# Kernel tuning notes

Measured on AMD Instinct MI355X. Metric: run time of the kernel, lower is better.

Reference implementation:

```python
import jax, jax.numpy as jnp
import numpy as np

IMG = 224          # image_size
FMAP = (56, 56)    # feature_map_dims (AdaptiveAvgPool2d((56,56)))
K_REWEIGHT = 3     # self.n_reweight
BLUR_RADIUS = 4    # KNNGaussianBlur(4): kernel 9, sigma 4


def _cdist(a, b):
    # Euclidean pairwise distance, [Na, D] x [Nb, D] -> [Na, Nb]
    a2 = jnp.sum(a * a, axis=1, keepdims=True)            # [Na,1]
    b2 = jnp.sum(b * b, axis=1, keepdims=True).T          # [1,Nb]
    d2 = a2 + b2 - 2.0 * (a @ b.T)
    return jnp.sqrt(jnp.maximum(d2, 0.0))


def _gaussian_blur(x):
    # x: [1,1,H,W]; torchvision GaussianBlur(kernel=9, sigma=4), reflect pad
    r, sigma = BLUR_RADIUS, float(BLUR_RADIUS)
    t = jnp.arange(2 * r + 1, dtype=x.dtype) - r
    g = jnp.exp(-(t * t) / (2.0 * sigma * sigma))
    g = g / jnp.sum(g)
    k2d = jnp.outer(g, g)[None, None]                     # [1,1,9,9]
    xp = jnp.pad(x, ((0, 0), (0, 0), (r, r), (r, r)), mode='reflect')
    return jax.lax.conv_general_dilated(
        xp, k2d, window_strides=(1, 1), padding='VALID',
        dimension_numbers=('NCHW', 'OIHW', 'NCHW'))


def setup_inputs() -> dict:
    key = jax.random.key(0)
    k1, k2 = jax.random.split(key)
    patch = jax.random.normal(k1, (FMAP[0] * FMAP[1], 768), dtype=jnp.float32)
    patch_lib = jax.random.normal(k2, (16384, 768), dtype=jnp.float32)
    mean = jnp.zeros((), dtype=jnp.float32)
    std = jnp.ones((), dtype=jnp.float32)
    return {"patch": patch, "patch_lib": patch_lib, "mean": mean, "std": std}


def reference(patch, patch_lib, mean, std):
    # normalization (method_name != 'Point_MAE' branch)
    p = (patch - mean) / std                               # [N, D]

    dist = _cdist(p, patch_lib)                            # [N, Nlib]
    min_val = jnp.min(dist, axis=1)                        # [N]
    min_idx = jnp.argmin(dist, axis=1)                     # [N]
    s_idx = jnp.argmax(min_val)
    s_star = jnp.max(min_val)

    m_test = p[s_idx]                                      # [D]
    m_star = patch_lib[min_idx[s_idx]]                     # [D]

    # distances of m_star to whole bank, k smallest
    w_dist = jnp.sqrt(jnp.maximum(
        jnp.sum((patch_lib - m_star) ** 2, axis=1), 0.0))  # [Nlib]
    _, nn_idx = jax.lax.top_k(-w_dist, K_REWEIGHT)         # smallest k
    m_star_knn = jnp.linalg.norm(
        m_test[None, :] - patch_lib[nn_idx[1:]], axis=1)   # [k-1]

    D_sqrt = jnp.sqrt(jnp.asarray(patch.shape[1], dtype=p.dtype))
    w = 1.0 - jnp.exp(s_star / D_sqrt) / jnp.sum(jnp.exp(m_star_knn / D_sqrt))
    s = w * s_star

    s_map = min_val.reshape(1, 1, *FMAP)
    s_map = jax.image.resize(s_map, (1, 1, IMG, IMG), method='bilinear')
    s_map = _gaussian_blur(s_map)
    return s, s_map
```

## Files before the change

### kernel.cpp

```cpp
#include <hip/hip_runtime.h>
#include <hip/hip_bf16.h>
#include <stdint.h>

#define N_PATCH 3136
#define N_PATCH_PAD 3200
#define N_LIB   16384
#define DIM     768
#define IMGSZ   224
#define FM      56

#define BK 32
#define KT 24
#define MT 25
#define NTILES 128

typedef __bf16 bf16_t;
typedef __bf16 bf16x8 __attribute__((ext_vector_type(8)));
typedef __bf16 bf16x4_v __attribute__((ext_vector_type(4)));
typedef float  f32x4  __attribute__((ext_vector_type(4)));

#define FLT_MAX_ 3.402823466e+38f

struct Scal {
  unsigned long long approx_max_pack;
  unsigned long long cand_pack[64];
  int cand[64];
  int cand_count;
  int done1;
};

__device__ __forceinline__ float wave_reduce_sum(float v) {
#pragma unroll
  for (int s = 32; s > 0; s >>= 1) v += __shfl_xor(v, s, 64);
  return v;
}

__device__ __forceinline__ unsigned long long shfl_xor_u64(unsigned long long v, int mask) {
  unsigned lo = (unsigned)v, hi = (unsigned)(v >> 32);
  lo = __shfl_xor(lo, mask, 64);
  hi = __shfl_xor(hi, mask, 64);
  return ((unsigned long long)hi << 32) | lo;
}

__device__ __forceinline__ void async16(const bf16_t* g, bf16_t* l) {
  __builtin_amdgcn_global_load_lds(
      (const __attribute__((address_space(1))) unsigned int*)g,
      (__attribute__((address_space(3))) unsigned int*)l, 16, 0, 0);
}

__global__ void prep_kernel(const float* __restrict__ patch, const float* __restrict__ lib,
                            const float* __restrict__ meanp, const float* __restrict__ stdp,
                            bf16_t* __restrict__ pb, bf16_t* __restrict__ lb,
                            float* __restrict__ a2, float* __restrict__ b2, Scal* sc) {
  int t = threadIdx.x;
  int lane = t & 63;
  if (blockIdx.x == 0) {
    if (t < 64) sc->cand_pack[t] = ~0ULL;
    if (t == 64) { sc->approx_max_pack = 0ULL; sc->cand_count = 0; sc->done1 = 0; }
  }
  if (blockIdx.x < N_PATCH / 4) {
    int row = blockIdx.x * 4 + (t >> 6);
    float mu = meanp[0], sd = stdp[0];
    float acc = 0.f;
#pragma unroll
    for (int k = 0; k < 3; k++) {
      float4 v = ((const float4*)(patch + (size_t)row * DIM))[lane + 64 * k];
      v.x = (v.x - mu) / sd; v.y = (v.y - mu) / sd;
      v.z = (v.z - mu) / sd; v.w = (v.w - mu) / sd;
      bf16x4_v o = {(__bf16)v.x, (__bf16)v.y, (__bf16)v.z, (__bf16)v.w};
      *(bf16x4_v*)(pb + (size_t)row * DIM + (lane + 64 * k) * 4) = o;
      acc += v.x*v.x + v.y*v.y + v.z*v.z + v.w*v.w;
    }
    acc = wave_reduce_sum(acc);
    if (lane == 0) a2[row] = acc;
  } else {
    int row = (blockIdx.x - N_PATCH / 4) * 4 + (t >> 6);
    float acc = 0.f;
#pragma unroll
    for (int k = 0; k < 3; k++) {
      float4 v = ((const float4*)(lib + (size_t)row * DIM))[lane + 64 * k];
      bf16x4_v o = {(__bf16)v.x, (__bf16)v.y, (__bf16)v.z, (__bf16)v.w};
      *(bf16x4_v*)(lb + (size_t)row * DIM + (lane + 64 * k) * 4) = o;
      acc += v.x*v.x + v.y*v.y + v.z*v.z + v.w*v.w;
    }
    acc = wave_reduce_sum(acc);
    if (lane == 0) b2[row] = acc;
  }
}

__global__ __launch_bounds__(256, 3)
void gemm_min_kernel(const bf16_t* __restrict__ pb, const bf16_t* __restrict__ lb,
                     const float* __restrict__ a2, const float* __restrict__ b2,
                     float* __restrict__ part) {
  __shared__ __align__(16) bf16_t As[2][128 * BK];
  __shared__ __align__(16) bf16_t Bs[2][128 * BK];
  __shared__ unsigned smin[128];

  const int t = threadIdx.x;
  const int wave = t >> 6;
  const int lane = t & 63;
  const int l15 = lane & 15;
  const int quad = lane >> 4;
  const int wm = (wave >> 1) * 64;
  const int wn = (wave & 1) * 64;

  const int lid = blockIdx.x;
  const int xcd = lid & 7;
  const int slot = lid >> 3;
  const int ntile = xcd + 8 * (slot / MT);
  const int mtile = slot % MT;
  const int m0 = mtile * 128;
  const int n0 = ntile * 128;

  int ra0 = m0 + (t >> 2);       if (ra0 > N_PATCH - 1) ra0 = N_PATCH - 1;
  int ra1 = m0 + 64 + (t >> 2);  if (ra1 > N_PATCH - 1) ra1 = N_PATCH - 1;
  const bf16_t* gA0 = pb + (size_t)ra0 * DIM + (t & 3) * 8;
  const bf16_t* gA1 = pb + (size_t)ra1 * DIM + (t & 3) * 8;
  const bf16_t* gB0 = lb + (size_t)(n0 + (t >> 2)) * DIM + (t & 3) * 8;
  const bf16_t* gB1 = gB0 + (size_t)64 * DIM;

  if (t < 128) smin[t] = 0xffffffffu;

  {
    bf16_t* la = &As[0][0];
    bf16_t* lb_ = &Bs[0][0];
    async16(gA0, la + t * 8);
    async16(gA1, la + 2048 + t * 8);
    async16(gB0, lb_ + t * 8);
    async16(gB1, lb_ + 2048 + t * 8);
  }
  __syncthreads();

  f32x4 acc[4][4];
#pragma unroll
  for (int mi = 0; mi < 4; mi++)
#pragma unroll
    for (int ni = 0; ni < 4; ni++) { f32x4 z = {0.f,0.f,0.f,0.f}; acc[mi][ni] = z; }

  for (int k = 0; k < KT; ++k) {
    const int cur = k & 1;
    if (k + 1 < KT) {
      const int nxt = cur ^ 1;
      const size_t ko = (size_t)(k + 1) * BK;
      bf16_t* la = &As[nxt][0];
      bf16_t* lb_ = &Bs[nxt][0];
      async16(gA0 + ko, la + t * 8);
      async16(gA1 + ko, la + 2048 + t * 8);
      async16(gB0 + ko, lb_ + t * 8);
      async16(gB1 + ko, lb_ + 2048 + t * 8);
    }

    bf16x8 afr[4], bfr[4];
#pragma unroll
    for (int mi = 0; mi < 4; mi++)
      afr[mi] = *(const bf16x8*)(&As[cur][(wm + mi * 16 + l15) * BK + quad * 8]);
#pragma unroll
    for (int ni = 0; ni < 4; ni++)
      bfr[ni] = *(const bf16x8*)(&Bs[cur][(wn + ni * 16 + l15) * BK + quad * 8]);
#pragma unroll
    for (int mi = 0; mi < 4; mi++)
#pragma unroll
      for (int ni = 0; ni < 4; ni++)
        acc[mi][ni] = __builtin_amdgcn_mfma_f32_16x16x32_bf16(afr[mi], bfr[ni],
                                                              acc[mi][ni], 0, 0, 0);
    __syncthreads();
  }

  float b2n[4];
#pragma unroll
  for (int ni = 0; ni < 4; ni++) b2n[ni] = b2[n0 + wn + ni * 16 + l15];

#pragma unroll
  for (int mi = 0; mi < 4; mi++) {
#pragma unroll
    for (int r = 0; r < 4; r++) {
      int rloc = wm + mi * 16 + quad * 4 + r;
      int mrow = m0 + rloc;
      float a2v = a2[mrow < N_PATCH ? mrow : (N_PATCH - 1)];
      float best = a2v + b2n[0] - 2.0f * acc[mi][0][r];
#pragma unroll
      for (int ni = 1; ni < 4; ni++)
        best = fminf(best, a2v + b2n[ni] - 2.0f * acc[mi][ni][r]);
      best = fmaxf(best, 0.0f);
#pragma unroll
      for (int s = 1; s < 16; s <<= 1)
        best = fminf(best, __shfl_xor(best, s, 64));
      if (l15 == 0) atomicMin(&smin[rloc], __float_as_uint(best));
    }
  }
  __syncthreads();
  if (t < 128) part[(size_t)ntile * N_PATCH_PAD + m0 + t] = __uint_as_float(smin[t]);
}

__global__ void finalize_collect_kernel(const float* __restrict__ part,
                                        float* __restrict__ min_val, Scal* sc) {
  __shared__ bool last;
  int t = threadIdx.x;
  int row = blockIdx.x * 128 + t;
  float m = FLT_MAX_;
#pragma unroll 8
  for (int nt = 0; nt < NTILES; nt++)
    m = fminf(m, part[(size_t)nt * N_PATCH_PAD + row]);
  if (row < N_PATCH) {
    float v = sqrtf(m);
    min_val[row] = v;
    unsigned long long mp = (((unsigned long long)__float_as_uint(v)) << 32) |
                            (unsigned)(0xffffffffu - (unsigned)row);
    atomicMax(&sc->approx_max_pack, mp);
  }
  __threadfence();
  __syncthreads();
  if (t == 0) last = (atomicAdd(&sc->done1, 1) == MT - 1);
  __syncthreads();
  if (!last) return;
  __threadfence();
  float amax = __uint_as_float((unsigned)(atomicMax(&sc->approx_max_pack, 0ULL) >> 32));
  for (int i = t; i < N_PATCH; i += 128) {
    if (min_val[i] >= amax - 0.02f) {
      int p = atomicAdd(&sc->cand_count, 1);
      if (p < 64) sc->cand[p] = i;
    }
  }
}

__global__ void refine_kernel(const float* __restrict__ patch, const float* __restrict__ lib,
                              const float* __restrict__ meanp, const float* __restrict__ stdp,
                              Scal* sc) {
  int c = blockIdx.x;
  int cnt = sc->cand_count; if (cnt > 64) cnt = 64;
  if (c >= cnt) return;
  int row = sc->cand[c];
  int wave = threadIdx.x >> 6, lane = threadIdx.x & 63;
  float mu = meanp[0], sd = stdp[0];
  float4 pv[3];
#pragma unroll
  for (int k = 0; k < 3; k++) {
    float4 v = ((const float4*)(patch + (size_t)row * DIM))[lane + 64 * k];
    v.x = (v.x - mu) / sd; v.y = (v.y - mu) / sd;
    v.z = (v.z - mu) / sd; v.w = (v.w - mu) / sd;
    pv[k] = v;
  }
  unsigned long long best = ~0ULL;
  int jbase = blockIdx.y * 128 + wave * 32;
  for (int rr = 0; rr < 32; rr++) {
    int j = jbase + rr;
    const float4* pl = (const float4*)(lib + (size_t)j * DIM);
    float acc = 0.f;
#pragma unroll
    for (int k = 0; k < 3; k++) {
      float4 l = pl[lane + 64 * k];
      float dx = pv[k].x - l.x, dy = pv[k].y - l.y;
      float dz = pv[k].z - l.z, dw = pv[k].w - l.w;
      acc += dx*dx + dy*dy + dz*dz + dw*dw;
    }
    acc = wave_reduce_sum(acc);
    unsigned long long pk = (((unsigned long long)__float_as_uint(acc)) << 32) | (unsigned)j;
    if (pk < best) best = pk;
  }
  if (lane == 0) atomicMin(&sc->cand_pack[c], best);
}

__device__ __forceinline__ void wave_pick(const Scal* sc, int lane,
                                          int* srow, float* sstar, int* ms) {
  int cnt = sc->cand_count; if (cnt > 64) cnt = 64;
  unsigned long long pk = 0ULL;
  int rowv = 0, msv = 0;
  if (lane < cnt) {
    unsigned long long cp = sc->cand_pack[lane];
    rowv = sc->cand[lane];
    msv = (int)(cp & 0xffffffffu);
    pk = (cp & 0xffffffff00000000ULL) | (unsigned)(0xffffffffu - (unsigned)rowv);
  }
  unsigned long long m = pk;
#pragma unroll
  for (int s = 1; s < 64; s <<= 1) {
    unsigned long long o = shfl_xor_u64(m, s);
    if (o > m) m = o;
  }
  unsigned long long mask = __ballot(pk == m && lane < cnt);
  int wl = (int)(__ffsll((long long)mask) - 1);
  *srow = __shfl(rowv, wl, 64);
  *ms   = __shfl(msv, wl, 64);
  *sstar = sqrtf(__uint_as_float((unsigned)(m >> 32)));
}

__global__ void wdist_kernel(const float* __restrict__ lib, const Scal* __restrict__ sc,
                             float* __restrict__ wdist2) {
  int wave = threadIdx.x >> 6, lane = threadIdx.x & 63;
  int srow_, ms; float ss_;
  wave_pick(sc, lane, &srow_, &ss_, &ms);
  float4 pm[3];
#pragma unroll
  for (int k = 0; k < 3; k++)
    pm[k] = ((const float4*)(lib + (size_t)ms * DIM))[lane + 64 * k];
  int jbase = blockIdx.x * 64 + wave * 16;
  for (int rr = 0; rr < 16; rr++) {
    int j = jbase + rr;
    const float4* pj = (const float4*)(lib + (size_t)j * DIM);
    float acc = 0.f;
#pragma unroll
    for (int k = 0; k < 3; k++) {
      float4 a = pj[lane + 64 * k];
      float dx = a.x - pm[k].x, dy = a.y - pm[k].y;
      float dz = a.z - pm[k].z, dw = a.w - pm[k].w;
      acc += dx*dx + dy*dy + dz*dz + dw*dw;
    }
    acc = wave_reduce_sum(acc);
    if (lane == 0) wdist2[j] = acc;
  }
}

__global__ void top3_kernel(const float* __restrict__ wdist2,
                            const float* __restrict__ patch, const float* __restrict__ lib,
                            const float* __restrict__ meanp, const float* __restrict__ stdp,
                            const Scal* __restrict__ sc, float* __restrict__ out) {
  __shared__ unsigned long long sl[768];
  int t = threadIdx.x;

  unsigned long long b0 = ~0ULL, b1 = ~0ULL, b2 = ~0ULL;
  for (int j = t; j < N_LIB; j += 256) {
    unsigned long long pk = (((unsigned long long)__float_as_uint(wdist2[j])) << 32) | (unsigned)j;
    if (pk < b0)      { b2 = b1; b1 = b0; b0 = pk; }
    else if (pk < b1) { b2 = b1; b1 = pk; }
    else if (pk < b2) { b2 = pk; }
  }
  sl[t * 3 + 0] = b0; sl[t * 3 + 1] = b1; sl[t * 3 + 2] = b2;
  __syncthreads();
  if (t >= 64) return;

  unsigned long long c0 = ~0ULL, c1 = ~0ULL, c2 = ~0ULL;
#pragma unroll
  for (int e = 0; e < 12; e++) {
    unsigned long long pk = sl[t * 12 + e];
    if (pk < c0)      { c2 = c1; c1 = c0; c0 = pk; }
    else if (pk < c1) { c2 = c1; c1 = pk; }
    else if (pk < c2) { c2 = pk; }
  }
  unsigned long long res1 = 0, res2 = 0;
#pragma unroll
  for (int r = 0; r < 3; r++) {
    unsigned long long m = c0;
#pragma unroll
    for (int s = 1; s < 64; s <<= 1) {
      unsigned long long o = shfl_xor_u64(m, s);
      if (o < m) m = o;
    }
    if (r == 1) res1 = m;
    if (r == 2) res2 = m;
    if (c0 == m) { c0 = c1; c1 = c2; c2 = ~0ULL; }
  }
  int nA = (int)(res1 & 0xffffffffu);
  int nB = (int)(res2 & 0xffffffffu);

  int srow, ms2; float sstar;
  wave_pick(sc, t, &srow, &sstar, &ms2);

  float mu = meanp[0], sd = stdp[0];
  float accA = 0.f, accB = 0.f;
#pragma unroll
  for (int k = 0; k < 3; k++) {
    float4 p4 = ((const float4*)(patch + (size_t)srow * DIM))[t + 64 * k];
    float4 a4 = ((const float4*)(lib + (size_t)nA * DIM))[t + 64 * k];
    float4 b4 = ((const float4*)(lib + (size_t)nB * DIM))[t + 64 * k];
    float px = (p4.x - mu) / sd, py = (p4.y - mu) / sd;
    float pz = (p4.z - mu) / sd, pw = (p4.w - mu) / sd;
    float dax = px - a4.x, day = py - a4.y, daz = pz - a4.z, daw = pw - a4.w;
    float dbx = px - b4.x, dby = py - b4.y, dbz = pz - b4.z, dbw = pw - b4.w;
    accA += dax*dax + day*day + daz*daz + daw*daw;
    accB += dbx*dbx + dby*dby + dbz*dbz + dbw*dbw;
  }
  accA = wave_reduce_sum(accA);
  accB = wave_reduce_sum(accB);
  if (t == 0) {
    float dsq = sqrtf((float)DIM);
    float d1 = sqrtf(accA), d2v = sqrtf(accB);
    float w = 1.0f - expf(sstar / dsq) / (expf(d1 / dsq) + expf(d2v / dsq));
    out[0] = w * sstar;
  }
}

__global__ void resize_blur_kernel(const float* __restrict__ mv, float* __restrict__ out) {
  __shared__ float rs[40 * 40];
  int bx = blockIdx.x % 7, by = blockIdx.x / 7;
  int ox0 = bx * 32, oy0 = by * 32;
  int t = threadIdx.x;

  for (int i = t; i < 1600; i += 256) {
    int ly = i / 40, lx = i % 40;
    int gy = oy0 - 4 + ly; gy = gy < 0 ? 0 : (gy > 223 ? 223 : gy);
    int gx = ox0 - 4 + lx; gx = gx < 0 ? 0 : (gx > 223 ? 223 : gx);
    float sy = fminf(fmaxf(0.25f * gy - 0.375f, 0.0f), 55.0f);
    float sx = fminf(fmaxf(0.25f * gx - 0.375f, 0.0f), 55.0f);
    int y0 = (int)sy; if (y0 > 54) y0 = 54;
    int x0 = (int)sx; if (x0 > 54) x0 = 54;
    float fy = sy - y0, fx = sx - x0;
    float v00 = mv[y0*FM + x0],     v01 = mv[y0*FM + x0 + 1];
    float v10 = mv[(y0+1)*FM + x0], v11 = mv[(y0+1)*FM + x0 + 1];
    float a = v00 + fx * (v01 - v00);
    float b = v10 + fx * (v11 - v10);
    rs[i] = a + fy * (b - a);
  }
  __syncthreads();

  float g[9]; float gs = 0.f;
#pragma unroll
  for (int i = 0; i < 9; i++) { float tt = (float)(i - 4); g[i] = expf(-(tt*tt)/32.0f); gs += g[i]; }
#pragma unroll
  for (int i = 0; i < 9; i++) g[i] /= gs;

  for (int p = t; p < 1024; p += 256) {
    int y = oy0 + p / 32, x = ox0 + (p & 31);
    float acc = 0.f;
#pragma unroll
    for (int dy = 0; dy < 9; dy++) {
      int yy = y + dy - 4;
      yy = yy < 0 ? -yy : (yy > IMGSZ - 1 ? 2*(IMGSZ-1) - yy : yy);
      int lyy = yy - (oy0 - 4);
      float ra = 0.f;
#pragma unroll
      for (int dx = 0; dx < 9; dx++) {
        int xx = x + dx - 4;
        xx = xx < 0 ? -xx : (xx > IMGSZ - 1 ? 2*(IMGSZ-1) - xx : xx);
        ra += g[dx] * rs[lyy * 40 + (xx - (ox0 - 4))];
      }
      acc += g[dy] * ra;
    }
    out[y * IMGSZ + x] = acc;
  }
}

extern "C" void kernel_launch(void* const* d_in, const int* in_sizes, int n_in,
                              void* d_out, int out_size, void* d_ws, size_t ws_size,
                              hipStream_t stream) {
  const float* patch = (const float*)d_in[0];
  const float* lib   = (const float*)d_in[1];
  const float* meanp = (const float*)d_in[2];
  const float* stdp  = (const float*)d_in[3];
  float* out = (float*)d_out;

  char* ws = (char*)d_ws;
  size_t off = 0;
  auto alloc = [&](size_t bytes) -> void* {
    void* p = ws + off;
    off = (off + bytes + 255) & ~(size_t)255;
    return p;
  };
  bf16_t* pb      = (bf16_t*)alloc((size_t)N_PATCH * DIM * sizeof(bf16_t));
  bf16_t* lb      = (bf16_t*)alloc((size_t)N_LIB * DIM * sizeof(bf16_t));
  float* a2       = (float*)alloc(N_PATCH * sizeof(float));
  float* b2       = (float*)alloc(N_LIB * sizeof(float));
  float* part     = (float*)alloc((size_t)N_PATCH_PAD * NTILES * sizeof(float));
  float* min_val  = (float*)alloc(N_PATCH * sizeof(float));
  float* wdist2   = (float*)alloc(N_LIB * sizeof(float));
  Scal*  sc       = (Scal*)alloc(sizeof(Scal));

  prep_kernel<<<N_PATCH / 4 + N_LIB / 4, 256, 0, stream>>>(patch, lib, meanp, stdp,
                                                           pb, lb, a2, b2, sc);
  gemm_min_kernel<<<MT * NTILES, 256, 0, stream>>>(pb, lb, a2, b2, part);
  finalize_collect_kernel<<<MT, 128, 0, stream>>>(part, min_val, sc);
  refine_kernel<<<dim3(64, 128), 256, 0, stream>>>(patch, lib, meanp, stdp, sc);
  wdist_kernel<<<256, 256, 0, stream>>>(lib, sc, wdist2);
  top3_kernel<<<1, 256, 0, stream>>>(wdist2, patch, lib, meanp, stdp, sc, out);
  resize_blur_kernel<<<49, 256, 0, stream>>>(min_val, out + 1);
}
```

Baseline: 367.5 us.

## Fuse post-GEMM tail kernels into one persistent kernel with grid barriers

Replaces five separate tail launches (finalize/collect, refine, wdist, top3, resize+blur) with a single 64-block kernel. The stages are separated by atomic-counter grid barriers kept in the Scal struct, whose counters prep_kernel resets. This targets the per-launch and inter-kernel gap overhead of the small tail stages. In exchange, the refine and wdist scans run on only 64 blocks instead of thousands or 256, which lowers memory-level parallelism for the library sweeps. Correctness relies on all 64 blocks being co-resident.

```diff
diff --git a/kernel.cpp b/kernel.cpp
--- a/kernel.cpp
+++ b/kernel.cpp
@@ -14,6 +14,8 @@
 #define MT 25
 #define NTILES 128
 
+#define TAILB 64
+
 typedef __bf16 bf16_t;
 typedef __bf16 bf16x8 __attribute__((ext_vector_type(8)));
 typedef __bf16 bf16x4_v __attribute__((ext_vector_type(4)));
@@ -26,7 +28,7 @@
   unsigned long long cand_pack[64];
   int cand[64];
   int cand_count;
-  int done1;
+  int bar[4];
 };
 
 __device__ __forceinline__ float wave_reduce_sum(float v) {
@@ -46,6 +48,17 @@
   __builtin_amdgcn_global_load_lds(
       (const __attribute__((address_space(1))) unsigned int*)g,
       (__attribute__((address_space(3))) unsigned int*)l, 16, 0, 0);
+}
+
+__device__ __forceinline__ void grid_bar(int* ctr, int nb) {
+  __syncthreads();
+  if (threadIdx.x == 0) {
+    __threadfence();
+    atomicAdd(ctr, 1);
+    while (atomicAdd(ctr, 0) < nb) __builtin_amdgcn_s_sleep(8);
+    __threadfence();
+  }
+  __syncthreads();
 }
 
 __global__ void prep_kernel(const float* __restrict__ patch, const float* __restrict__ lib,
@@ -56,7 +69,8 @@
   int lane = t & 63;
   if (blockIdx.x == 0) {
     if (t < 64) sc->cand_pack[t] = ~0ULL;
-    if (t == 64) { sc->approx_max_pack = 0ULL; sc->cand_count = 0; sc->done1 = 0; }
+    if (t == 64) { sc->approx_max_pack = 0ULL; sc->cand_count = 0; }
+    if (t >= 65 && t < 69) sc->bar[t - 65] = 0;
   }
   if (blockIdx.x < N_PATCH / 4) {
     int row = blockIdx.x * 4 + (t >> 6);
@@ -192,77 +206,8 @@
   if (t < 128) part[(size_t)ntile * N_PATCH_PAD + m0 + t] = __uint_as_float(smin[t]);
 }
 
-__global__ void finalize_collect_kernel(const float* __restrict__ part,
-                                        float* __restrict__ min_val, Scal* sc) {
-  __shared__ bool last;
-  int t = threadIdx.x;
-  int row = blockIdx.x * 128 + t;
-  float m = FLT_MAX_;
-#pragma unroll 8
-  for (int nt = 0; nt < NTILES; nt++)
-    m = fminf(m, part[(size_t)nt * N_PATCH_PAD + row]);
-  if (row < N_PATCH) {
-    float v = sqrtf(m);
-    min_val[row] = v;
-    unsigned long long mp = (((unsigned long long)__float_as_uint(v)) << 32) |
-                            (unsigned)(0xffffffffu - (unsigned)row);
-    atomicMax(&sc->approx_max_pack, mp);
-  }
-  __threadfence();
-  __syncthreads();
-  if (t == 0) last = (atomicAdd(&sc->done1, 1) == MT - 1);
-  __syncthreads();
-  if (!last) return;
-  __threadfence();
-  float amax = __uint_as_float((unsigned)(atomicMax(&sc->approx_max_pack, 0ULL) >> 32));
-  for (int i = t; i < N_PATCH; i += 128) {
-    if (min_val[i] >= amax - 0.02f) {
-      int p = atomicAdd(&sc->cand_count, 1);
-      if (p < 64) sc->cand[p] = i;
-    }
-  }
-}
-
-__global__ void refine_kernel(const float* __restrict__ patch, const float* __restrict__ lib,
-                              const float* __restrict__ meanp, const float* __restrict__ stdp,
-                              Scal* sc) {
-  int c = blockIdx.x;
-  int cnt = sc->cand_count; if (cnt > 64) cnt = 64;
-  if (c >= cnt) return;
-  int row = sc->cand[c];
-  int wave = threadIdx.x >> 6, lane = threadIdx.x & 63;
-  float mu = meanp[0], sd = stdp[0];
-  float4 pv[3];
-#pragma unroll
-  for (int k = 0; k < 3; k++) {
-    float4 v = ((const float4*)(patch + (size_t)row * DIM))[lane + 64 * k];
-    v.x = (v.x - mu) / sd; v.y = (v.y - mu) / sd;
-    v.z = (v.z - mu) / sd; v.w = (v.w - mu) / sd;
-    pv[k] = v;
-  }
-  unsigned long long best = ~0ULL;
-  int jbase = blockIdx.y * 128 + wave * 32;
-  for (int rr = 0; rr < 32; rr++) {
-    int j = jbase + rr;
-    const float4* pl = (const float4*)(lib + (size_t)j * DIM);
-    float acc = 0.f;
-#pragma unroll
-    for (int k = 0; k < 3; k++) {
-      float4 l = pl[lane + 64 * k];
-      float dx = pv[k].x - l.x, dy = pv[k].y - l.y;
-      float dz = pv[k].z - l.z, dw = pv[k].w - l.w;
-      acc += dx*dx + dy*dy + dz*dz + dw*dw;
-    }
-    acc = wave_reduce_sum(acc);
-    unsigned long long pk = (((unsigned long long)__float_as_uint(acc)) << 32) | (unsigned)j;
-    if (pk < best) best = pk;
-  }
-  if (lane == 0) atomicMin(&sc->cand_pack[c], best);
-}
-
-__device__ __forceinline__ void wave_pick(const Scal* sc, int lane,
+__device__ __forceinline__ void wave_pick(const Scal* sc, int cnt, int lane,
                                           int* srow, float* sstar, int* ms) {
-  int cnt = sc->cand_count; if (cnt > 64) cnt = 64;
   unsigned long long pk = 0ULL;
   int rowv = 0, msv = 0;
   if (lane < cnt) {
@@ -284,148 +229,224 @@
   *sstar = sqrtf(__uint_as_float((unsigned)(m >> 32)));
 }
 
-__global__ void wdist_kernel(const float* __restrict__ lib, const Scal* __restrict__ sc,
-                             float* __restrict__ wdist2) {
-  int wave = threadIdx.x >> 6, lane = threadIdx.x & 63;
-  int srow_, ms; float ss_;
-  wave_pick(sc, lane, &srow_, &ss_, &ms);
-  float4 pm[3];
-#pragma unroll
-  for (int k = 0; k < 3; k++)
-    pm[k] = ((const float4*)(lib + (size_t)ms * DIM))[lane + 64 * k];
-  int jbase = blockIdx.x * 64 + wave * 16;
-  for (int rr = 0; rr < 16; rr++) {
-    int j = jbase + rr;
-    const float4* pj = (const float4*)(lib + (size_t)j * DIM);
-    float acc = 0.f;
+__global__ __launch_bounds__(256, 2)
+void tail_kernel(const float* __restrict__ part, float* __restrict__ min_val,
+                 const float* __restrict__ patch, const float* __restrict__ lib,
+                 const float* __restrict__ meanp, const float* __restrict__ stdp,
+                 Scal* __restrict__ sc, float* __restrict__ wdist2,
+                 float* __restrict__ out0, float* __restrict__ outmap) {
+  __shared__ union {
+    unsigned long long sl[768];
+    float rs[40 * 40];
+  } sm;
+  __shared__ int s_cnt;
+
+  const int t = threadIdx.x;
+  const int b = blockIdx.x;
+  const int wave = t >> 6, lane = t & 63;
+
+  {
+    int row = b * 256 + t;
+    if (row < N_PATCH) {
+      float m = FLT_MAX_;
+#pragma unroll 8
+      for (int nt = 0; nt < NTILES; nt++)
+        m = fminf(m, part[(size_t)nt * N_PATCH_PAD + row]);
+      float v = sqrtf(m);
+      min_val[row] = v;
+      unsigned long long mp = (((unsigned long long)__float_as_uint(v)) << 32) |
+                              (unsigned)(0xffffffffu - (unsigned)row);
+      atomicMax(&sc->approx_max_pack, mp);
+    }
+  }
+  grid_bar(&sc->bar[0], TAILB);
+
+  if (b == 0) {
+    float amax = __uint_as_float((unsigned)(atomicMax(&sc->approx_max_pack, 0ULL) >> 32));
+    for (int i = t; i < N_PATCH; i += 256) {
+      if (min_val[i] >= amax - 0.02f) {
+        int p = atomicAdd(&sc->cand_count, 1);
+        if (p < 64) sc->cand[p] = i;
+      }
+    }
+  }
+  grid_bar(&sc->bar[1], TAILB);
+
+  if (t == 0) s_cnt = atomicAdd(&sc->cand_count, 0);
+  __syncthreads();
+  int cnt = s_cnt; if (cnt > 64) cnt = 64;
+
+  {
+    float mu = meanp[0], sd = stdp[0];
+    for (int c = 0; c < cnt; c++) {
+      int row = sc->cand[c];
+      float4 pv[3];
+#pragma unroll
+      for (int k = 0; k < 3; k++) {
+        float4 v = ((const float4*)(patch + (size_t)row * DIM))[lane + 64 * k];
+        v.x = (v.x - mu) / sd; v.y = (v.y - mu) / sd;
+        v.z = (v.z - mu) / sd; v.w = (v.w - mu) / sd;
+        pv[k] = v;
+      }
+      unsigned long long best = ~0ULL;
+      int jbase = b * 256 + wave * 64;
+      for (int rr = 0; rr < 64; rr++) {
+        int j = jbase + rr;
+        const float4* pl = (const float4*)(lib + (size_t)j * DIM);
+        float acc = 0.f;
+#pragma unroll
+        for (int k = 0; k < 3; k++) {
+          float4 l = pl[lane + 64 * k];
+          float dx = pv[k].x - l.x, dy = pv[k].y - l.y;
+          float dz = pv[k].z - l.z, dw = pv[k].w - l.w;
+          acc += dx*dx + dy*dy + dz*dz + dw*dw;
+        }
+        acc = wave_reduce_sum(acc);
+        unsigned long long pk = (((unsigned long long)__float_as_uint(acc)) << 32) | (unsigned)j;
+        if (pk < best) best = pk;
+      }
+      if (lane == 0) atomicMin(&sc->cand_pack[c], best);
+    }
+  }
+  grid_bar(&sc->bar[2], TAILB);
+
+  {
+    int srow_, ms; float ss_;
+    wave_pick(sc, cnt, lane, &srow_, &ss_, &ms);
+    float4 pm[3];
+#pragma unroll
+    for (int k = 0; k < 3; k++)
+      pm[k] = ((const float4*)(lib + (size_t)ms * DIM))[lane + 64 * k];
+    int jbase = b * 256 + wave * 64;
+    for (int rr = 0; rr < 64; rr++) {
+      int j = jbase + rr;
+      const float4* pj = (const float4*)(lib + (size_t)j * DIM);
+      float acc = 0.f;
+#pragma unroll
+      for (int k = 0; k < 3; k++) {
+        float4 a = pj[lane + 64 * k];
+        float dx = a.x - pm[k].x, dy = a.y - pm[k].y;
+        float dz = a.z - pm[k].z, dw = a.w - pm[k].w;
+        acc += dx*dx + dy*dy + dz*dz + dw*dw;
+      }
+      acc = wave_reduce_sum(acc);
+      if (lane == 0) wdist2[j] = acc;
+    }
+  }
+  grid_bar(&sc->bar[3], TAILB);
+
+  if (b == 0) {
+    unsigned long long b0 = ~0ULL, b1 = ~0ULL, b2 = ~0ULL;
+    for (int j = t; j < N_LIB; j += 256) {
+      unsigned long long pk = (((unsigned long long)__float_as_uint(wdist2[j])) << 32) | (unsigned)j;
+      if (pk < b0)      { b2 = b1; b1 = b0; b0 = pk; }
+      else if (pk < b1) { b2 = b1; b1 = pk; }
+      else if (pk < b2) { b2 = pk; }
+    }
+    sm.sl[t * 3 + 0] = b0; sm.sl[t * 3 + 1] = b1; sm.sl[t * 3 + 2] = b2;
+    __syncthreads();
+    if (t >= 64) return;
+
+    unsigned long long c0 = ~0ULL, c1 = ~0ULL, c2 = ~0ULL;
+#pragma unroll
+    for (int e = 0; e < 12; e++) {
+      unsigned long long pk = sm.sl[t * 12 + e];
+      if (pk < c0)      { c2 = c1; c1 = c0; c0 = pk; }
+      else if (pk < c1) { c2 = c1; c1 = pk; }
+      else if (pk < c2) { c2 = pk; }
+    }
+    unsigned long long res1 = 0, res2 = 0;
+#pragma unroll
+    for (int r = 0; r < 3; r++) {
+      unsigned long long m = c0;
+#pragma unroll
+      for (int s = 1; s < 64; s <<= 1) {
+        unsigned long long o = shfl_xor_u64(m, s);
+        if (o < m) m = o;
+      }
+      if (r == 1) res1 = m;
+      if (r == 2) res2 = m;
+      if (c0 == m) { c0 = c1; c1 = c2; c2 = ~0ULL; }
+    }
+    int nA = (int)(res1 & 0xffffffffu);
+    int nB = (int)(res2 & 0xffffffffu);
+
+    int srow, ms2; float sstar;
+    wave_pick(sc, cnt, t, &srow, &sstar, &ms2);
+
+    float mu = meanp[0], sd = stdp[0];
+    float accA = 0.f, accB = 0.f;
 #pragma unroll
     for (int k = 0; k < 3; k++) {
-      float4 a = pj[lane + 64 * k];
-      float dx = a.x - pm[k].x, dy = a.y - pm[k].y;
-      float dz = a.z - pm[k].z, dw = a.w - pm[k].w;
-      acc += dx*dx + dy*dy + dz*dz + dw*dw;
-    }
-    acc = wave_reduce_sum(acc);
-    if (lane == 0) wdist2[j] = acc;
-  }
-}
-
-__global__ void top3_kernel(const float* __restrict__ wdist2,
-                            const float* __restrict__ patch, const float* __restrict__ lib,
-                            const float* __restrict__ meanp, const float* __restrict__ stdp,
-                            const Scal* __restrict__ sc, float* __restrict__ out) {
-  __shared__ unsigned long long sl[768];
-  int t = threadIdx.x;
-
-  unsigned long long b0 = ~0ULL, b1 = ~0ULL, b2 = ~0ULL;
-  for (int j = t; j < N_LIB; j += 256) {
-    unsigned long long pk = (((unsigned long long)__float_as_uint(wdist2[j])) << 32) | (unsigned)j;
-    if (pk < b0)      { b2 = b1; b1 = b0; b0 = pk; }
-    else if (pk < b1) { b2 = b1; b1 = pk; }
-    else if (pk < b2) { b2 = pk; }
-  }
-  sl[t * 3 + 0] = b0; sl[t * 3 + 1] = b1; sl[t * 3 + 2] = b2;
-  __syncthreads();
-  if (t >= 64) return;
-
-  unsigned long long c0 = ~0ULL, c1 = ~0ULL, c2 = ~0ULL;
-#pragma unroll
-  for (int e = 0; e < 12; e++) {
-    unsigned long long pk = sl[t * 12 + e];
-    if (pk < c0)      { c2 = c1; c1 = c0; c0 = pk; }
-    else if (pk < c1) { c2 = c1; c1 = pk; }
-    else if (pk < c2) { c2 = pk; }
-  }
-  unsigned long long res1 = 0, res2 = 0;
-#pragma unroll
-  for (int r = 0; r < 3; r++) {
-    unsigned long long m = c0;
-#pragma unroll
-    for (int s = 1; s < 64; s <<= 1) {
-      unsigned long long o = shfl_xor_u64(m, s);
-      if (o < m) m = o;
-    }
-    if (r == 1) res1 = m;
-    if (r == 2) res2 = m;
-    if (c0 == m) { c0 = c1; c1 = c2; c2 = ~0ULL; }
-  }
-  int nA = (int)(res1 & 0xffffffffu);
-  int nB = (int)(res2 & 0xffffffffu);
-
-  int srow, ms2; float sstar;
-  wave_pick(sc, t, &srow, &sstar, &ms2);
-
-  float mu = meanp[0], sd = stdp[0];
-  float accA = 0.f, accB = 0.f;
-#pragma unroll
-  for (int k = 0; k < 3; k++) {
-    float4 p4 = ((const float4*)(patch + (size_t)srow * DIM))[t + 64 * k];
-    float4 a4 = ((const float4*)(lib + (size_t)nA * DIM))[t + 64 * k];
-    float4 b4 = ((const float4*)(lib + (size_t)nB * DIM))[t + 64 * k];
-    float px = (p4.x - mu) / sd, py = (p4.y - mu) / sd;
-    float pz = (p4.z - mu) / sd, pw = (p4.w - mu) / sd;
-    float dax = px - a4.x, day = py - a4.y, daz = pz - a4.z, daw = pw - a4.w;
-    float dbx = px - b4.x, dby = py - b4.y, dbz = pz - b4.z, dbw = pw - b4.w;
-    accA += dax*dax + day*day + daz*daz + daw*daw;
-    accB += dbx*dbx + dby*dby + dbz*dbz + dbw*dbw;
-  }
-  accA = wave_reduce_sum(accA);
-  accB = wave_reduce_sum(accB);
-  if (t == 0) {
-    float dsq = sqrtf((float)DIM);
-    float d1 = sqrtf(accA), d2v = sqrtf(accB);
-    float w = 1.0f - expf(sstar / dsq) / (expf(d1 / dsq) + expf(d2v / dsq));
-    out[0] = w * sstar;
-  }
-}
-
-__global__ void resize_blur_kernel(const float* __restrict__ mv, float* __restrict__ out) {
-  __shared__ float rs[40 * 40];
-  int bx = blockIdx.x % 7, by = blockIdx.x / 7;
-  int ox0 = bx * 32, oy0 = by * 32;
-  int t = threadIdx.x;
-
-  for (int i = t; i < 1600; i += 256) {
-    int ly = i / 40, lx = i % 40;
-    int gy = oy0 - 4 + ly; gy = gy < 0 ? 0 : (gy > 223 ? 223 : gy);
-    int gx = ox0 - 4 + lx; gx = gx < 0 ? 0 : (gx > 223 ? 223 : gx);
-    float sy = fminf(fmaxf(0.25f * gy - 0.375f, 0.0f), 55.0f);
-    float sx = fminf(fmaxf(0.25f * gx - 0.375f, 0.0f), 55.0f);
-    int y0 = (int)sy; if (y0 > 54) y0 = 54;
-    int x0 = (int)sx; if (x0 > 54) x0 = 54;
-    float fy = sy - y0, fx = sx - x0;
-    float v00 = mv[y0*FM + x0],     v01 = mv[y0*FM + x0 + 1];
-    float v10 = mv[(y0+1)*FM + x0], v11 = mv[(y0+1)*FM + x0 + 1];
-    float a = v00 + fx * (v01 - v00);
-    float b = v10 + fx * (v11 - v10);
-    rs[i] = a + fy * (b - a);
-  }
-  __syncthreads();
-
-  float g[9]; float gs = 0.f;
-#pragma unroll
-  for (int i = 0; i < 9; i++) { float tt = (float)(i - 4); g[i] = expf(-(tt*tt)/32.0f); gs += g[i]; }
-#pragma unroll
-  for (int i = 0; i < 9; i++) g[i] /= gs;
-
-  for (int p = t; p < 1024; p += 256) {
-    int y = oy0 + p / 32, x = ox0 + (p & 31);
-    float acc = 0.f;
-#pragma unroll
-    for (int dy = 0; dy < 9; dy++) {
-      int yy = y + dy - 4;
-      yy = yy < 0 ? -yy : (yy > IMGSZ - 1 ? 2*(IMGSZ-1) - yy : yy);
-      int lyy = yy - (oy0 - 4);
-      float ra = 0.f;
-#pragma unroll
-      for (int dx = 0; dx < 9; dx++) {
-        int xx = x + dx - 4;
-        xx = xx < 0 ? -xx : (xx > IMGSZ - 1 ? 2*(IMGSZ-1) - xx : xx);
-        ra += g[dx] * rs[lyy * 40 + (xx - (ox0 - 4))];
-      }
-      acc += g[dy] * ra;
-    }
-    out[y * IMGSZ + x] = acc;
+      float4 p4 = ((const float4*)(patch + (size_t)srow * DIM))[t + 64 * k];
+      float4 a4 = ((const float4*)(lib + (size_t)nA * DIM))[t + 64 * k];
+      float4 b4 = ((const float4*)(lib + (size_t)nB * DIM))[t + 64 * k];
+      float px = (p4.x - mu) / sd, py = (p4.y - mu) / sd;
+      float pz = (p4.z - mu) / sd, pw = (p4.w - mu) / sd;
+      float dax = px - a4.x, day = py - a4.y, daz = pz - a4.z, daw = pw - a4.w;
+      float dbx = px - b4.x, dby = py - b4.y, dbz = pz - b4.z, dbw = pw - b4.w;
+      accA += dax*dax + day*day + daz*daz + daw*daw;
+      accB += dbx*dbx + dby*dby + dbz*dbz + dbw*dbw;
+    }
+    accA = wave_reduce_sum(accA);
+    accB = wave_reduce_sum(accB);
+    if (t == 0) {
+      float dsq = sqrtf((float)DIM);
+      float d1 = sqrtf(accA), d2v = sqrtf(accB);
+      float w = 1.0f - expf(sstar / dsq) / (expf(d1 / dsq) + expf(d2v / dsq));
+      out0[0] = w * sstar;
+    }
+    return;
+  }
+
+  if (b > 49) return;
+  {
+    int tile = b - 1;
+    int bx = tile % 7, by = tile / 7;
+    int ox0 = bx * 32, oy0 = by * 32;
+
+    for (int i = t; i < 1600; i += 256) {
+      int ly = i / 40, lx = i % 40;
+      int gy = oy0 - 4 + ly; gy = gy < 0 ? 0 : (gy > 223 ? 223 : gy);
+      int gx = ox0 - 4 + lx; gx = gx < 0 ? 0 : (gx > 223 ? 223 : gx);
+      float sy = fminf(fmaxf(0.25f * gy - 0.375f, 0.0f), 55.0f);
+      float sx = fminf(fmaxf(0.25f * gx - 0.375f, 0.0f), 55.0f);
+      int y0 = (int)sy; if (y0 > 54) y0 = 54;
+      int x0 = (int)sx; if (x0 > 54) x0 = 54;
+      float fy = sy - y0, fx = sx - x0;
+      float v00 = min_val[y0*FM + x0],     v01 = min_val[y0*FM + x0 + 1];
+      float v10 = min_val[(y0+1)*FM + x0], v11 = min_val[(y0+1)*FM + x0 + 1];
+      float a = v00 + fx * (v01 - v00);
+      float bb = v10 + fx * (v11 - v10);
+      sm.rs[i] = a + fy * (bb - a);
+    }
+    __syncthreads();
+
+    float g[9]; float gs = 0.f;
+#pragma unroll
+    for (int i = 0; i < 9; i++) { float tt = (float)(i - 4); g[i] = expf(-(tt*tt)/32.0f); gs += g[i]; }
+#pragma unroll
+    for (int i = 0; i < 9; i++) g[i] /= gs;
+
+    for (int p = t; p < 1024; p += 256) {
+      int y = oy0 + p / 32, x = ox0 + (p & 31);
+      float acc = 0.f;
+#pragma unroll
+      for (int dy = 0; dy < 9; dy++) {
+        int yy = y + dy - 4;
+        yy = yy < 0 ? -yy : (yy > IMGSZ - 1 ? 2*(IMGSZ-1) - yy : yy);
+        int lyy = yy - (oy0 - 4);
+        float ra = 0.f;
+#pragma unroll
+        for (int dx = 0; dx < 9; dx++) {
+          int xx = x + dx - 4;
+          xx = xx < 0 ? -xx : (xx > IMGSZ - 1 ? 2*(IMGSZ-1) - xx : xx);
+          ra += g[dx] * sm.rs[lyy * 40 + (xx - (ox0 - 4))];
+        }
+        acc += g[dy] * ra;
+      }
+      outmap[y * IMGSZ + x] = acc;
+    }
   }
 }
 
@@ -457,9 +478,6 @@
   prep_kernel<<<N_PATCH / 4 + N_LIB / 4, 256, 0, stream>>>(patch, lib, meanp, stdp,
                                                            pb, lb, a2, b2, sc);
   gemm_min_kernel<<<MT * NTILES, 256, 0, stream>>>(pb, lb, a2, b2, part);
-  finalize_collect_kernel<<<MT, 128, 0, stream>>>(part, min_val, sc);
-  refine_kernel<<<dim3(64, 128), 256, 0, stream>>>(patch, lib, meanp, stdp, sc);
-  wdist_kernel<<<256, 256, 0, stream>>>(lib, sc, wdist2);
-  top3_kernel<<<1, 256, 0, stream>>>(wdist2, patch, lib, meanp, stdp, sc, out);
-  resize_blur_kernel<<<49, 256, 0, stream>>>(min_val, out + 1);
-}
+  tail_kernel<<<TAILB, 256, 0, stream>>>(part, min_val, patch, lib, meanp, stdp,
+                                         sc, wdist2, out, out + 1);
+}
```

New measurement: 353.6 us. 3.8% less time.
